# Optimization experiments

Hardware: AMD Instinct MI355X
Metric: run time of the kernel (lower is better)

Reference implementation:

```python
import jax, jax.numpy as jnp
import numpy as np

N_GROUP = 8
TOPK_GROUP = 4
TOP_K = 8
ROUTED_SCALING_FACTOR = 2.5


def setup_inputs() -> dict:
    key = jax.random.key(0)
    ks = jax.random.split(key, 6)
    T, H, I, E = 256, 1024, 512, 32
    x = jax.random.normal(ks[0], (T, H), dtype=jnp.float32)
    gate_w = jax.random.normal(ks[1], (H, E), dtype=jnp.float32) * 0.05
    e_score_bias = jax.random.normal(ks[2], (E,), dtype=jnp.float32) * 0.05
    Wg = jax.random.normal(ks[3], (E, H, I), dtype=jnp.float32) * 0.02
    Wu = jax.random.normal(ks[4], (E, H, I), dtype=jnp.float32) * 0.02
    Wd = jax.random.normal(ks[5], (E, I, H), dtype=jnp.float32) * 0.02
    return {"x": x, "gate_w": gate_w, "e_score_bias": e_score_bias,
            "Wg": Wg, "Wu": Wu, "Wd": Wd}


def _route_ds3(x, gate_w, e_score_bias):
    # DeepSeek-V3 group-limited top-k routing (routing_ds3 in source).
    T = x.shape[0]
    E = gate_w.shape[1]
    logits = x @ gate_w                      # [T, E]
    scores = jax.nn.sigmoid(logits)
    scores_for_choice = scores + e_score_bias[None, :]
    gsz = E // N_GROUP
    grouped = scores_for_choice.reshape(T, N_GROUP, gsz)
    # group score = sum of top-2 expert scores in group
    group_scores = jnp.sum(jax.lax.top_k(grouped, 2)[0], axis=-1)     # [T, n_group]
    _, group_idx = jax.lax.top_k(group_scores, TOPK_GROUP)            # [T, topk_group]
    rows = jnp.arange(T)[:, None]
    group_mask = jnp.zeros((T, N_GROUP), scores.dtype).at[rows, group_idx].set(1.0)
    score_mask = jnp.repeat(group_mask, gsz, axis=-1)                 # [T, E]
    masked = jnp.where(score_mask > 0, scores_for_choice, 0.0)
    _, topk_idx = jax.lax.top_k(masked, TOP_K)                        # [T, k]
    topk_w = jnp.take_along_axis(scores, topk_idx, axis=1)            # gather raw scores
    topk_w = topk_w / (jnp.sum(topk_w, axis=-1, keepdims=True) + 1e-20)
    topk_w = topk_w * ROUTED_SCALING_FACTOR
    return topk_idx, topk_w


def reference(x, gate_w, e_score_bias, Wg, Wu, Wd):
    T = x.shape[0]
    E = gate_w.shape[1]
    topk_idx, topk_w = _route_ds3(x, gate_w, e_score_bias)
    # dense [T, E] routing-weight matrix (topk indices are unique per row)
    rows = jnp.arange(T)[:, None]
    rw = jnp.zeros((T, E), x.dtype).at[rows, topk_idx].set(topk_w)
    # expert gated MLP (silu), combined with routing weights
    g = jnp.einsum('th,ehi->tei', x, Wg)      # [T, E, I]
    u = jnp.einsum('th,ehi->tei', x, Wu)
    a = jax.nn.silu(g) * u
    y = jnp.einsum('tei,eih->teh', a, Wd)     # [T, E, H]
    out = jnp.einsum('te,teh->th', rw, y)     # weighted combine
    return out
```

## Files before the change

kernel.cpp:

```cpp
#include <hip/hip_runtime.h>
#include <cstdint>
#include <cmath>

constexpr int TT   = 256;
constexpr int HD   = 1024;
constexpr int IDIM = 512;
constexpr int NE   = 32;
constexpr int NGRP = 8;
constexpr int TKG  = 4;
constexpr int TOPK = 8;
constexpr float RSCALE = 2.5f;

constexpr int NSX  = HD / 32;
constexpr int NSA  = IDIM / 32;
constexpr int SLAB = 16 * 64 * 8;

typedef float    f32x4 __attribute__((ext_vector_type(4)));
typedef _Float16 half8 __attribute__((ext_vector_type(8)));

constexpr size_t WS_CNT = 0;
constexpr size_t WS_TOK = 256;
constexpr size_t WS_WL  = WS_TOK + (size_t)NE * TT * 4;
constexpr size_t WS_XE  = WS_WL  + (size_t)NE * TT * 4;
constexpr size_t WS_A   = WS_XE  + (size_t)NE * NSX * SLAB * 2;

#define GLOAD16(GP, LP) __builtin_amdgcn_global_load_lds(                      \
    (const __attribute__((address_space(1))) unsigned int*)(GP),               \
    (__attribute__((address_space(3))) unsigned int*)(LP), 16, 0, 0)

#define WAITVM(N) asm volatile("s_waitcnt vmcnt(" #N ")" ::: "memory")

__global__ __launch_bounds__(256) void k_route(
    const float* __restrict__ x, const float* __restrict__ gw,
    const float* __restrict__ bias, int* __restrict__ cnt,
    int* __restrict__ tok, float* __restrict__ wl)
{
    int t = blockIdx.x;
    int tid = threadIdx.x;
    int e2 = (tid & 15) * 2;
    int c  = tid >> 4;
    const float* xr = x + (size_t)t * HD;

    float a0 = 0.f, a1 = 0.f;
    int h0 = c * (HD / 16);
#pragma unroll 8
    for (int h = h0; h < h0 + HD / 16; ++h) {
        float xv = xr[h];
        float2 wv = *(const float2*)&gw[(size_t)h * NE + e2];
        a0 += xv * wv.x;
        a1 += xv * wv.y;
    }

    __shared__ float part[16][NE];
    part[c][e2]     = a0;
    part[c][e2 + 1] = a1;
    __syncthreads();

    __shared__ float sc[NE], sfc[NE];
    if (tid < NE) {
        float s = 0.f;
#pragma unroll
        for (int cc = 0; cc < 16; ++cc) s += part[cc][tid];
        float sig = 1.f / (1.f + expf(-s));
        sc[tid]  = sig;
        sfc[tid] = sig + bias[tid];
    }
    __syncthreads();

    if (tid == 0) {
        float gs[NGRP];
        for (int g = 0; g < NGRP; ++g) {
            float m1 = -3.0e38f, m2 = -3.0e38f;
            for (int j = 0; j < 4; ++j) {
                float v = sfc[4 * g + j];
                if (v > m1) { m2 = m1; m1 = v; } else if (v > m2) m2 = v;
            }
            gs[g] = m1 + m2;
        }
        bool gsel[NGRP];
        for (int g = 0; g < NGRP; ++g) gsel[g] = false;
        for (int r = 0; r < TKG; ++r) {
            int bi = -1; float bv = -3.0e38f;
            for (int g = 0; g < NGRP; ++g)
                if (!gsel[g] && gs[g] > bv) { bv = gs[g]; bi = g; }
            gsel[bi] = true;
        }
        float masked[NE];
        for (int i = 0; i < NE; ++i) masked[i] = gsel[i >> 2] ? sfc[i] : 0.0f;
        int   idx[TOPK]; float wv[TOPK]; float wsum = 0.f;
        for (int r = 0; r < TOPK; ++r) {
            int bi = -1; float bv = -3.0e38f;
            for (int i = 0; i < NE; ++i)
                if (masked[i] > bv) { bv = masked[i]; bi = i; }
            masked[bi] = -3.0e38f;
            idx[r] = bi; wv[r] = sc[bi]; wsum += wv[r];
        }
        float inv = RSCALE / (wsum + 1e-20f);
        for (int r = 0; r < TOPK; ++r) {
            int ee = idx[r];
            int pos = atomicAdd(&cnt[ee], 1);
            tok[(size_t)ee * TT + pos] = t;
            wl [(size_t)ee * TT + pos] = wv[r] * inv;
        }
    }
}

__global__ __launch_bounds__(256) void k_pack(
    const float* __restrict__ x, const int* __restrict__ cnt,
    const int* __restrict__ tok, _Float16* __restrict__ Xe)
{
    int bid  = blockIdx.x;
    int xcd  = bid & 7;
    int slot = bid >> 3;
    int e    = xcd * 4 + (slot & 3);
    int s    = slot >> 2;
    int n_e = cnt[e];
    if (n_e == 0) return;
    int tid = threadIdx.x, w = tid >> 6, lane = tid & 63;
    int m16 = lane & 15, q = lane >> 4;
    _Float16* base = Xe + ((size_t)e * NSX + s) * SLAB;
#pragma unroll
    for (int k = 0; k < 4; ++k) {
        int mt = w + k * 4;
        int slot2 = mt * 16 + m16;
        if (slot2 >= n_e) slot2 = n_e - 1;
        int t = tok[e * TT + slot2];
        const float* src = x + (size_t)t * HD + s * 32 + q * 8;
        f32x4 v0 = *(const f32x4*)src;
        f32x4 v1 = *(const f32x4*)(src + 4);
        half8 h;
        h[0] = (_Float16)v0.x; h[1] = (_Float16)v0.y; h[2] = (_Float16)v0.z; h[3] = (_Float16)v0.w;
        h[4] = (_Float16)v1.x; h[5] = (_Float16)v1.y; h[6] = (_Float16)v1.z; h[7] = (_Float16)v1.w;
        *(half8*)(base + ((size_t)mt * 64 + lane) * 8) = h;
    }
}

__global__ __launch_bounds__(128, 1) void k_gateup(
    const _Float16* __restrict__ Xe, const float* __restrict__ Wg,
    const float* __restrict__ Wu, const int* __restrict__ cnt,
    _Float16* __restrict__ A)
{
    int bid  = blockIdx.x;
    int xcd  = bid & 7;
    int slot = bid >> 3;
    int e    = xcd * 4 + (slot & 3);
    int rest = slot >> 2;
    int ttile = rest & 1;
    int ig    = rest >> 1;
    int n_e = cnt[e];
    if (ttile * 128 >= n_e) return;
    int mtbase = ttile * 8;
    int i0 = ig * 32;
    int tid  = threadIdx.x;
    int w    = tid >> 6;
    int lane = tid & 63;
    int m16 = lane & 15, q = lane >> 4;
    int wcol = w * 16 + m16;

    __shared__ __align__(16) float LG[6][32][32];
    __shared__ __align__(16) float LU[6][32][32];

    const _Float16* abase = Xe + (size_t)e * NSX * SLAB + ((size_t)mtbase * 64 + lane) * 8;
    const float* gw0 = Wg + (size_t)e * HD * IDIM + i0;
    const float* uw0 = Wu + (size_t)e * HD * IDIM + i0;

    f32x4 accG[8], accU[8];
#pragma unroll
    for (int mt = 0; mt < 8; ++mt) {
        accG[mt] = (f32x4){0.f, 0.f, 0.f, 0.f};
        accU[mt] = (f32x4){0.f, 0.f, 0.f, 0.f};
    }

    half8 af[3][8];

#define GU_STAGE(B, KS)                                                        \
    { _Pragma("unroll")                                                        \
      for (int ci = 0; ci < 2; ++ci) {                                         \
        int c    = w * 2 + ci;                                                 \
        int row  = c * 8 + (lane >> 3);                                        \
        int csrc = ((lane & 7) << 2) ^ ((c & 1) << 4);                         \
        const float* gs = gw0 + ((size_t)(KS) * 32 + row) * IDIM + csrc;       \
        const float* us = uw0 + ((size_t)(KS) * 32 + row) * IDIM + csrc;       \
        GLOAD16(gs, &LG[B][c * 8][0]);                                         \
        GLOAD16(us, &LU[B][c * 8][0]);                                         \
      } }

#define GU_LOADA(KS, AF)                                                       \
    { const _Float16* a_ = abase + (size_t)(KS) * SLAB;                        \
      _Pragma("unroll")                                                        \
      for (int mt_ = 0; mt_ < 8; ++mt_) AF[mt_] = *(const half8*)(a_ + mt_ * 512); }

#define GU_COMPUTE(B, AF)                                                      \
    { int lc = wcol ^ ((q & 1) << 4);                                          \
      half8 bg, bu;                                                            \
      _Pragma("unroll")                                                        \
      for (int j_ = 0; j_ < 8; ++j_) {                                         \
        bg[j_] = (_Float16)LG[B][q * 8 + j_][lc];                              \
        bu[j_] = (_Float16)LU[B][q * 8 + j_][lc];                              \
      }                                                                        \
      _Pragma("unroll")                                                        \
      for (int mt_ = 0; mt_ < 8; ++mt_) {                                      \
        accG[mt_] = __builtin_amdgcn_mfma_f32_16x16x32_f16(AF[mt_], bg, accG[mt_], 0, 0, 0); \
        accU[mt_] = __builtin_amdgcn_mfma_f32_16x16x32_f16(AF[mt_], bu, accU[mt_], 0, 0, 0); \
      } }

    constexpr int NK = HD / 32;
    GU_STAGE(0, 0) GU_STAGE(1, 1) GU_STAGE(2, 2) GU_STAGE(3, 3)
    GU_LOADA(0, af[0]) GU_LOADA(1, af[1])

#pragma unroll
    for (int ks = 0; ks < NK; ++ks) {
        if (ks + 4 < NK) GU_STAGE((ks + 4) % 6, ks + 4)
        if (ks + 2 < NK) GU_LOADA(ks + 2, af[(ks + 2) % 3])
        if      (ks == 0)      { WAITVM(20); }
        else if (ks + 5 <= NK) { WAITVM(24); }
        else if (ks + 4 == NK) { WAITVM(20); }
        else if (ks + 3 == NK) { WAITVM(16); }
        else if (ks + 2 == NK) { WAITVM(8);  }
        else                   { WAITVM(0);  }
        __builtin_amdgcn_s_barrier();
        __builtin_amdgcn_sched_barrier(0);
        GU_COMPUTE(ks % 6, af[ks % 3])
    }
#undef GU_STAGE
#undef GU_LOADA
#undef GU_COMPUTE

    int iyw = ig * 2 + w;
    _Float16* aout = A + ((size_t)e * NSA + (iyw >> 1)) * SLAB;
    int cj   = m16 & 7;
    int lsub = ((iyw * 2 + (m16 >> 3)) & 3) * 16;
#pragma unroll
    for (int mt = 0; mt < 8; ++mt) {
#pragma unroll
        for (int r = 0; r < 4; ++r) {
            float g = accG[mt][r], u = accU[mt][r];
            float a = (g / (1.f + expf(-g))) * u;
            int lp = (q * 4 + r) + lsub;
            aout[((size_t)(mtbase + mt) * 64 + lp) * 8 + cj] = (_Float16)a;
        }
    }
}

__global__ __launch_bounds__(128, 1) void k_down(
    const _Float16* __restrict__ A, const float* __restrict__ Wd,
    const int* __restrict__ cnt, const int* __restrict__ tok,
    const float* __restrict__ wl, float* __restrict__ outf)
{
    int bid  = blockIdx.x;
    int xcd  = bid & 7;
    int slot = bid >> 3;
    int e    = xcd * 4 + (slot & 3);
    int rest = slot >> 2;
    int ttile = rest & 1;
    int hg    = rest >> 1;
    int n_e = cnt[e];
    if (ttile * 128 >= n_e) return;
    int mtbase = ttile * 8;
    int h0 = hg * 32;
    int tid  = threadIdx.x;
    int w    = tid >> 6;
    int lane = tid & 63;
    int m16 = lane & 15, q = lane >> 4;
    int wcol = w * 16 + m16;

    __shared__ __align__(16) float LD[6][32][32];

    const _Float16* abase = A + (size_t)e * NSA * SLAB + ((size_t)mtbase * 64 + lane) * 8;
    const float* dw0 = Wd + (size_t)e * IDIM * HD + h0;

    f32x4 acc[8];
#pragma unroll
    for (int mt = 0; mt < 8; ++mt) acc[mt] = (f32x4){0.f, 0.f, 0.f, 0.f};

    half8 af[3][8];

#define DN_STAGE(B, KS)                                                        \
    { _Pragma("unroll")                                                        \
      for (int ci = 0; ci < 2; ++ci) {                                         \
        int c    = w * 2 + ci;                                                 \
        int row  = c * 8 + (lane >> 3);                                        \
        int csrc = ((lane & 7) << 2) ^ ((c & 1) << 4);                         \
        const float* ds = dw0 + ((size_t)(KS) * 32 + row) * HD + csrc;         \
        GLOAD16(ds, &LD[B][c * 8][0]);                                         \
      } }

#define DN_LOADA(KS, AF)                                                       \
    { const _Float16* a_ = abase + (size_t)(KS) * SLAB;                        \
      _Pragma("unroll")                                                        \
      for (int mt_ = 0; mt_ < 8; ++mt_) AF[mt_] = *(const half8*)(a_ + mt_ * 512); }

#define DN_COMPUTE(B, AF)                                                      \
    { int lc = wcol ^ ((q & 1) << 4);                                          \
      half8 bd;                                                                \
      _Pragma("unroll")                                                        \
      for (int j_ = 0; j_ < 8; ++j_) bd[j_] = (_Float16)LD[B][q * 8 + j_][lc]; \
      _Pragma("unroll")                                                        \
      for (int mt_ = 0; mt_ < 8; ++mt_)                                        \
        acc[mt_] = __builtin_amdgcn_mfma_f32_16x16x32_f16(AF[mt_], bd, acc[mt_], 0, 0, 0); }

    constexpr int NK = IDIM / 32;
    DN_STAGE(0, 0) DN_STAGE(1, 1) DN_STAGE(2, 2) DN_STAGE(3, 3)
    DN_LOADA(0, af[0]) DN_LOADA(1, af[1])

#pragma unroll
    for (int ks = 0; ks < NK; ++ks) {
        if (ks + 4 < NK) DN_STAGE((ks + 4) % 6, ks + 4)
        if (ks + 2 < NK) DN_LOADA(ks + 2, af[(ks + 2) % 3])
        if      (ks == 0)      { WAITVM(18); }
        else if (ks + 5 <= NK) { WAITVM(20); }
        else if (ks + 4 == NK) { WAITVM(18); }
        else if (ks + 3 == NK) { WAITVM(16); }
        else if (ks + 2 == NK) { WAITVM(8);  }
        else                   { WAITVM(0);  }
        __builtin_amdgcn_s_barrier();
        __builtin_amdgcn_sched_barrier(0);
        DN_COMPUTE(ks % 6, af[ks % 3])
    }
#undef DN_STAGE
#undef DN_LOADA
#undef DN_COMPUTE

    int col = h0 + w * 16 + m16;
#pragma unroll
    for (int mt = 0; mt < 8; ++mt) {
#pragma unroll
        for (int r = 0; r < 4; ++r) {
            int slot2 = ttile * 128 + mt * 16 + q * 4 + r;
            if (slot2 < n_e) {
                int t   = tok[(size_t)e * TT + slot2];
                float wt = wl[(size_t)e * TT + slot2];
                atomicAdd(&outf[(size_t)t * HD + col], wt * acc[mt][r]);
            }
        }
    }
}

extern "C" void kernel_launch(void* const* d_in, const int* in_sizes, int n_in,
                              void* d_out, int out_size, void* d_ws, size_t ws_size,
                              hipStream_t stream) {
    const float* x    = (const float*)d_in[0];
    const float* gw   = (const float*)d_in[1];
    const float* bias = (const float*)d_in[2];
    const float* Wg   = (const float*)d_in[3];
    const float* Wu   = (const float*)d_in[4];
    const float* Wd   = (const float*)d_in[5];
    float* out = (float*)d_out;

    char* ws = (char*)d_ws;
    int*      cnt = (int*)(ws + WS_CNT);
    int*      tok = (int*)(ws + WS_TOK);
    float*    wl  = (float*)(ws + WS_WL);
    _Float16* Xe  = (_Float16*)(ws + WS_XE);
    _Float16* A   = (_Float16*)(ws + WS_A);

    hipMemsetAsync(ws, 0, 256, stream);
    hipMemsetAsync(out, 0, (size_t)TT * HD * 4, stream);

    k_route<<<TT, 256, 0, stream>>>(x, gw, bias, cnt, tok, wl);
    k_pack<<<NE * NSX, 256, 0, stream>>>(x, cnt, tok, Xe);
    k_gateup<<<NE * 2 * (IDIM / 32), 128, 0, stream>>>(Xe, Wg, Wu, cnt, A);
    k_down<<<NE * 2 * (HD / 32), 128, 0, stream>>>(A, Wd, cnt, tok, wl, out);
}
```

Measured before the change: 276.4 us.

## Stage A operand through LDS and replace atomic scatter with deterministic combine kernel

Both MoE GEMM kernels now load the fp16 activation slab into LDS with global_load_lds alongside the weight tiles, using a 5-stage ring instead of 6 weight stages plus register-prefetched A fragments. The down-projection no longer does atomicAdd into the output. It writes weighted per-slot rows into a compact Y buffer (reusing the Xe workspace), and a new combine kernel sums each token's 8 slots. This removes atomic contention and the output memset, and it frees VGPRs from the A prefetch. In exchange it adds two small kernel launches, an extra round-trip of Y through global memory, and more LDS per block.

```diff
diff --git a/kernel.cpp b/kernel.cpp
--- a/kernel.cpp
+++ b/kernel.cpp
@@ -18,11 +18,13 @@
 typedef float    f32x4 __attribute__((ext_vector_type(4)));
 typedef _Float16 half8 __attribute__((ext_vector_type(8)));
 
-constexpr size_t WS_CNT = 0;
-constexpr size_t WS_TOK = 256;
-constexpr size_t WS_WL  = WS_TOK + (size_t)NE * TT * 4;
-constexpr size_t WS_XE  = WS_WL  + (size_t)NE * TT * 4;
-constexpr size_t WS_A   = WS_XE  + (size_t)NE * NSX * SLAB * 2;
+constexpr size_t WS_CNT   = 0;
+constexpr size_t WS_TOK   = 256;
+constexpr size_t WS_WL    = WS_TOK   + (size_t)NE * TT * 4;
+constexpr size_t WS_TSLOT = WS_WL    + (size_t)NE * TT * 4;
+constexpr size_t WS_OFFS  = WS_TSLOT + (size_t)TT * TOPK * 4;
+constexpr size_t WS_XE    = WS_OFFS  + 256;
+constexpr size_t WS_A     = WS_XE + (size_t)NE * NSX * SLAB * 2;
 
 #define GLOAD16(GP, LP) __builtin_amdgcn_global_load_lds(                      \
     (const __attribute__((address_space(1))) unsigned int*)(GP),               \
@@ -33,7 +35,7 @@
 __global__ __launch_bounds__(256) void k_route(
     const float* __restrict__ x, const float* __restrict__ gw,
     const float* __restrict__ bias, int* __restrict__ cnt,
-    int* __restrict__ tok, float* __restrict__ wl)
+    int* __restrict__ tok, float* __restrict__ wl, int* __restrict__ tslot)
 {
     int t = blockIdx.x;
     int tid = threadIdx.x;
@@ -101,7 +103,17 @@
             int pos = atomicAdd(&cnt[ee], 1);
             tok[(size_t)ee * TT + pos] = t;
             wl [(size_t)ee * TT + pos] = wv[r] * inv;
-        }
+            tslot[t * TOPK + r] = ee * TT + pos;
+        }
+    }
+}
+
+__global__ __launch_bounds__(64) void k_offs(const int* __restrict__ cnt,
+                                             int* __restrict__ offs)
+{
+    if (threadIdx.x == 0) {
+        int s = 0;
+        for (int e = 0; e < NE; ++e) { offs[e] = s; s += cnt[e]; }
     }
 }
 
@@ -157,10 +169,11 @@
     int m16 = lane & 15, q = lane >> 4;
     int wcol = w * 16 + m16;
 
-    __shared__ __align__(16) float LG[6][32][32];
-    __shared__ __align__(16) float LU[6][32][32];
-
-    const _Float16* abase = Xe + (size_t)e * NSX * SLAB + ((size_t)mtbase * 64 + lane) * 8;
+    __shared__ __align__(16) float    LG[5][32][32];
+    __shared__ __align__(16) float    LU[5][32][32];
+    __shared__ __align__(16) _Float16 LA[5][4096];
+
+    const _Float16* aslab = Xe + (size_t)e * NSX * SLAB + (size_t)mtbase * 512;
     const float* gw0 = Wg + (size_t)e * HD * IDIM + i0;
     const float* uw0 = Wu + (size_t)e * HD * IDIM + i0;
 
@@ -170,8 +183,6 @@
         accG[mt] = (f32x4){0.f, 0.f, 0.f, 0.f};
         accU[mt] = (f32x4){0.f, 0.f, 0.f, 0.f};
     }
-
-    half8 af[3][8];
 
 #define GU_STAGE(B, KS)                                                        \
     { _Pragma("unroll")                                                        \
@@ -183,14 +194,15 @@
         const float* us = uw0 + ((size_t)(KS) * 32 + row) * IDIM + csrc;       \
         GLOAD16(gs, &LG[B][c * 8][0]);                                         \
         GLOAD16(us, &LU[B][c * 8][0]);                                         \
+      }                                                                        \
+      _Pragma("unroll")                                                        \
+      for (int i_ = 0; i_ < 4; ++i_) {                                         \
+        int off_ = (w * 4 + i_) * 512;                                         \
+        const _Float16* as_ = aslab + (size_t)(KS) * SLAB + off_ + lane * 8;   \
+        GLOAD16(as_, &LA[B][off_]);                                            \
       } }
 
-#define GU_LOADA(KS, AF)                                                       \
-    { const _Float16* a_ = abase + (size_t)(KS) * SLAB;                        \
-      _Pragma("unroll")                                                        \
-      for (int mt_ = 0; mt_ < 8; ++mt_) AF[mt_] = *(const half8*)(a_ + mt_ * 512); }
-
-#define GU_COMPUTE(B, AF)                                                      \
+#define GU_COMPUTE(B)                                                          \
     { int lc = wcol ^ ((q & 1) << 4);                                          \
       half8 bg, bu;                                                            \
       _Pragma("unroll")                                                        \
@@ -200,30 +212,26 @@
       }                                                                        \
       _Pragma("unroll")                                                        \
       for (int mt_ = 0; mt_ < 8; ++mt_) {                                      \
-        accG[mt_] = __builtin_amdgcn_mfma_f32_16x16x32_f16(AF[mt_], bg, accG[mt_], 0, 0, 0); \
-        accU[mt_] = __builtin_amdgcn_mfma_f32_16x16x32_f16(AF[mt_], bu, accU[mt_], 0, 0, 0); \
+        half8 afr = *(const half8*)&LA[B][mt_ * 512 + lane * 8];               \
+        accG[mt_] = __builtin_amdgcn_mfma_f32_16x16x32_f16(afr, bg, accG[mt_], 0, 0, 0); \
+        accU[mt_] = __builtin_amdgcn_mfma_f32_16x16x32_f16(afr, bu, accU[mt_], 0, 0, 0); \
       } }
 
     constexpr int NK = HD / 32;
-    GU_STAGE(0, 0) GU_STAGE(1, 1) GU_STAGE(2, 2) GU_STAGE(3, 3)
-    GU_LOADA(0, af[0]) GU_LOADA(1, af[1])
+    GU_STAGE(0, 0) GU_STAGE(1, 1) GU_STAGE(2, 2)
 
 #pragma unroll
     for (int ks = 0; ks < NK; ++ks) {
-        if (ks + 4 < NK) GU_STAGE((ks + 4) % 6, ks + 4)
-        if (ks + 2 < NK) GU_LOADA(ks + 2, af[(ks + 2) % 3])
-        if      (ks == 0)      { WAITVM(20); }
-        else if (ks + 5 <= NK) { WAITVM(24); }
-        else if (ks + 4 == NK) { WAITVM(20); }
+        if (ks + 3 < NK) GU_STAGE((ks + 3) % 5, ks + 3)
+        if      (ks + 4 <= NK) { WAITVM(24); }
         else if (ks + 3 == NK) { WAITVM(16); }
         else if (ks + 2 == NK) { WAITVM(8);  }
         else                   { WAITVM(0);  }
         __builtin_amdgcn_s_barrier();
         __builtin_amdgcn_sched_barrier(0);
-        GU_COMPUTE(ks % 6, af[ks % 3])
+        GU_COMPUTE(ks % 5)
     }
 #undef GU_STAGE
-#undef GU_LOADA
 #undef GU_COMPUTE
 
     int iyw = ig * 2 + w;
@@ -244,8 +252,8 @@
 
 __global__ __launch_bounds__(128, 1) void k_down(
     const _Float16* __restrict__ A, const float* __restrict__ Wd,
-    const int* __restrict__ cnt, const int* __restrict__ tok,
-    const float* __restrict__ wl, float* __restrict__ outf)
+    const int* __restrict__ cnt, const int* __restrict__ offs,
+    const float* __restrict__ wl, float* __restrict__ Y)
 {
     int bid  = blockIdx.x;
     int xcd  = bid & 7;
@@ -264,16 +272,15 @@
     int m16 = lane & 15, q = lane >> 4;
     int wcol = w * 16 + m16;
 
-    __shared__ __align__(16) float LD[6][32][32];
-
-    const _Float16* abase = A + (size_t)e * NSA * SLAB + ((size_t)mtbase * 64 + lane) * 8;
+    __shared__ __align__(16) float    LD[5][32][32];
+    __shared__ __align__(16) _Float16 LA[5][4096];
+
+    const _Float16* aslab = A + (size_t)e * NSA * SLAB + (size_t)mtbase * 512;
     const float* dw0 = Wd + (size_t)e * IDIM * HD + h0;
 
     f32x4 acc[8];
 #pragma unroll
     for (int mt = 0; mt < 8; ++mt) acc[mt] = (f32x4){0.f, 0.f, 0.f, 0.f};
-
-    half8 af[3][8];
 
 #define DN_STAGE(B, KS)                                                        \
     { _Pragma("unroll")                                                        \
@@ -283,44 +290,43 @@
         int csrc = ((lane & 7) << 2) ^ ((c & 1) << 4);                         \
         const float* ds = dw0 + ((size_t)(KS) * 32 + row) * HD + csrc;         \
         GLOAD16(ds, &LD[B][c * 8][0]);                                         \
+      }                                                                        \
+      _Pragma("unroll")                                                        \
+      for (int i_ = 0; i_ < 4; ++i_) {                                         \
+        int off_ = (w * 4 + i_) * 512;                                         \
+        const _Float16* as_ = aslab + (size_t)(KS) * SLAB + off_ + lane * 8;   \
+        GLOAD16(as_, &LA[B][off_]);                                            \
       } }
 
-#define DN_LOADA(KS, AF)                                                       \
-    { const _Float16* a_ = abase + (size_t)(KS) * SLAB;                        \
-      _Pragma("unroll")                                                        \
-      for (int mt_ = 0; mt_ < 8; ++mt_) AF[mt_] = *(const half8*)(a_ + mt_ * 512); }
-
-#define DN_COMPUTE(B, AF)                                                      \
+#define DN_COMPUTE(B)                                                          \
     { int lc = wcol ^ ((q & 1) << 4);                                          \
       half8 bd;                                                                \
       _Pragma("unroll")                                                        \
       for (int j_ = 0; j_ < 8; ++j_) bd[j_] = (_Float16)LD[B][q * 8 + j_][lc]; \
       _Pragma("unroll")                                                        \
-      for (int mt_ = 0; mt_ < 8; ++mt_)                                        \
-        acc[mt_] = __builtin_amdgcn_mfma_f32_16x16x32_f16(AF[mt_], bd, acc[mt_], 0, 0, 0); }
+      for (int mt_ = 0; mt_ < 8; ++mt_) {                                      \
+        half8 afr = *(const half8*)&LA[B][mt_ * 512 + lane * 8];               \
+        acc[mt_] = __builtin_amdgcn_mfma_f32_16x16x32_f16(afr, bd, acc[mt_], 0, 0, 0); \
+      } }
 
     constexpr int NK = IDIM / 32;
-    DN_STAGE(0, 0) DN_STAGE(1, 1) DN_STAGE(2, 2) DN_STAGE(3, 3)
-    DN_LOADA(0, af[0]) DN_LOADA(1, af[1])
+    DN_STAGE(0, 0) DN_STAGE(1, 1) DN_STAGE(2, 2)
 
 #pragma unroll
     for (int ks = 0; ks < NK; ++ks) {
-        if (ks + 4 < NK) DN_STAGE((ks + 4) % 6, ks + 4)
-        if (ks + 2 < NK) DN_LOADA(ks + 2, af[(ks + 2) % 3])
-        if      (ks == 0)      { WAITVM(18); }
-        else if (ks + 5 <= NK) { WAITVM(20); }
-        else if (ks + 4 == NK) { WAITVM(18); }
-        else if (ks + 3 == NK) { WAITVM(16); }
-        else if (ks + 2 == NK) { WAITVM(8);  }
+        if (ks + 3 < NK) DN_STAGE((ks + 3) % 5, ks + 3)
+        if      (ks + 4 <= NK) { WAITVM(18); }
+        else if (ks + 3 == NK) { WAITVM(12); }
+        else if (ks + 2 == NK) { WAITVM(6);  }
         else                   { WAITVM(0);  }
         __builtin_amdgcn_s_barrier();
         __builtin_amdgcn_sched_barrier(0);
-        DN_COMPUTE(ks % 6, af[ks % 3])
+        DN_COMPUTE(ks % 5)
     }
 #undef DN_STAGE
-#undef DN_LOADA
 #undef DN_COMPUTE
 
+    int oe = offs[e];
     int col = h0 + w * 16 + m16;
 #pragma unroll
     for (int mt = 0; mt < 8; ++mt) {
@@ -328,12 +334,29 @@
         for (int r = 0; r < 4; ++r) {
             int slot2 = ttile * 128 + mt * 16 + q * 4 + r;
             if (slot2 < n_e) {
-                int t   = tok[(size_t)e * TT + slot2];
                 float wt = wl[(size_t)e * TT + slot2];
-                atomicAdd(&outf[(size_t)t * HD + col], wt * acc[mt][r]);
+                Y[(size_t)(oe + slot2) * HD + col] = wt * acc[mt][r];
             }
         }
     }
+}
+
+__global__ __launch_bounds__(256) void k_combine(
+    const float* __restrict__ Y, const int* __restrict__ tslot,
+    const int* __restrict__ offs, float* __restrict__ out)
+{
+    int t = blockIdx.x, tid = threadIdx.x;
+    f32x4 s = (f32x4){0.f, 0.f, 0.f, 0.f};
+#pragma unroll
+    for (int r = 0; r < TOPK; ++r) {
+        int ts  = tslot[t * TOPK + r];
+        int e   = ts >> 8;
+        int pos = ts & 255;
+        const float* yp = Y + (size_t)(offs[e] + pos) * HD + tid * 4;
+        f32x4 v = *(const f32x4*)yp;
+        s.x += v.x; s.y += v.y; s.z += v.z; s.w += v.w;
+    }
+    *(f32x4*)&out[(size_t)t * HD + tid * 4] = s;
 }
 
 extern "C" void kernel_launch(void* const* d_in, const int* in_sizes, int n_in,
@@ -348,17 +371,21 @@
     float* out = (float*)d_out;
 
     char* ws = (char*)d_ws;
-    int*      cnt = (int*)(ws + WS_CNT);
-    int*      tok = (int*)(ws + WS_TOK);
-    float*    wl  = (float*)(ws + WS_WL);
-    _Float16* Xe  = (_Float16*)(ws + WS_XE);
-    _Float16* A   = (_Float16*)(ws + WS_A);
+    int*      cnt   = (int*)(ws + WS_CNT);
+    int*      tok   = (int*)(ws + WS_TOK);
+    float*    wl    = (float*)(ws + WS_WL);
+    int*      tslot = (int*)(ws + WS_TSLOT);
+    int*      offs  = (int*)(ws + WS_OFFS);
+    _Float16* Xe    = (_Float16*)(ws + WS_XE);
+    _Float16* A     = (_Float16*)(ws + WS_A);
+    float*    Y     = (float*)(ws + WS_XE);
 
     hipMemsetAsync(ws, 0, 256, stream);
-    hipMemsetAsync(out, 0, (size_t)TT * HD * 4, stream);
-
-    k_route<<<TT, 256, 0, stream>>>(x, gw, bias, cnt, tok, wl);
+
+    k_route<<<TT, 256, 0, stream>>>(x, gw, bias, cnt, tok, wl, tslot);
+    k_offs<<<1, 64, 0, stream>>>(cnt, offs);
     k_pack<<<NE * NSX, 256, 0, stream>>>(x, cnt, tok, Xe);
     k_gateup<<<NE * 2 * (IDIM / 32), 128, 0, stream>>>(Xe, Wg, Wu, cnt, A);
-    k_down<<<NE * 2 * (HD / 32), 128, 0, stream>>>(A, Wd, cnt, tok, wl, out);
-}
+    k_down<<<NE * 2 * (HD / 32), 128, 0, stream>>>(A, Wd, cnt, offs, wl, Y);
+    k_combine<<<TT, 256, 0, stream>>>(Y, tslot, offs, out);
+}
```

New measurement: 256.6 us. 1.08x faster.
